# Optimization experiments

Measured on AMD Instinct MI355X. Metric: run time of the kernel, lower is better.

## Reference

```python
import jax, jax.numpy as jnp
import numpy as np

B, CIN, COUT, K, IH, IW = 2, 32, 32, 9, 256, 256
OH, OW = 512, 512


def setup_inputs() -> dict:
    key = jax.random.key(0)
    k0, k1, k2, k3 = jax.random.split(key, 4)
    stdv = 1.0 / np.sqrt(CIN * K)
    x = jax.random.normal(k0, (B, CIN, IH, IW), jnp.float32)
    weight = jax.random.uniform(k1, (CIN, COUT, K), jnp.float32, -stdv, stdv)
    bias = jax.random.uniform(k2, (COUT,), jnp.float32, -stdv, stdv)
    # continuous (x, y) coords into the OUTPUT plane; keep strictly inside so x0+1/y0+1 are valid
    sm = jax.random.uniform(k3, (IH, IW, K, 2), jnp.float32)
    scale = jnp.array([(OW - 1) * 0.999, (OH - 1) * 0.999], jnp.float32)
    sample_map = sm * scale
    return {"x": x, "weight": weight, "bias": bias, "sample_map": sample_map, "oh": OH, "ow": OW}


def reference(x, weight, bias, sample_map, oh, ow):
    Bb, Cin, Ih, Iw = x.shape
    Cout = weight.shape[1]
    Kk = weight.shape[2]
    P = Ih * Iw
    xf = x.reshape(Bb, Cin, P)
    # per-kernel-tap weight transform of every input pixel: [B, Cout, K, P]
    contrib = jnp.einsum('bip,iok->bokp', xf, weight)

    sx = sample_map[..., 0].reshape(P, Kk).T  # [K, P] x-coords in output
    sy = sample_map[..., 1].reshape(P, Kk).T  # [K, P] y-coords in output
    x0f = jnp.floor(sx)
    y0f = jnp.floor(sy)
    dx = sx - x0f
    dy = sy - y0f
    x0 = jnp.clip(x0f.astype(jnp.int32), 0, ow - 1)
    y0 = jnp.clip(y0f.astype(jnp.int32), 0, oh - 1)
    x1 = jnp.clip(x0 + 1, 0, ow - 1)
    y1 = jnp.clip(y0 + 1, 0, oh - 1)

    # bilinear splat weights and flat output indices for the 4 corners: [4, K, P]
    w = jnp.stack([(1 - dx) * (1 - dy), dx * (1 - dy), (1 - dx) * dy, dx * dy], 0)
    idx = jnp.stack([y0 * ow + x0, y0 * ow + x1, y1 * ow + x0, y1 * ow + x1], 0)

    vals = contrib[:, :, None, :, :] * w[None, None, :, :, :]  # [B, Cout, 4, K, P]
    out = jnp.zeros((Bb, Cout, oh * ow), vals.dtype).at[:, :, idx].add(vals)
    return out.reshape(Bb, Cout, oh, ow) + bias[None, :, None, None]
```

## Files before the change

### kernel.cpp

```cpp
#include <hip/hip_runtime.h>
#include <hip/hip_fp16.h>

#define CIN 32
#define COUT 32
#define KK 9
#define PIX 65536
#define OH 512
#define OW 512
#define OHOW (OH*OW)
#define NCH 64
#define TW 16
#define TH 4
#define TPX (TW*TH)
#define NTX (OW/TW)
#define NTY (OH/TH)
#define NTILE (NTX*NTY)
#define NBIN NTILE
#define NPK (PIX*KK)
#define NSEG 4
#define SCAP 96
#define CAPT (NSEG*SCAP)

#define OFF_CNT 0
#define OFF_WT  (256*1024)
#define OFF_ENT (512*1024)
#define OFF_CB  (OFF_ENT + (size_t)NBIN*NSEG*SCAP*8)
#define WS_NEED (OFF_CB + (size_t)NPK*NCH*2)

typedef __bf16    bf16x8 __attribute__((ext_vector_type(8)));
typedef _Float16  f16x8  __attribute__((ext_vector_type(8)));
typedef float     f32x4  __attribute__((ext_vector_type(4)));

__device__ __forceinline__ unsigned short f2h(float v)
{
    return __half_as_ushort(__float2half_rn(v));
}

__device__ __forceinline__ void corners(float sx, float sy,
    int& x0, int& y0, int& x1, int& y1, float& dx, float& dy)
{
    const float x0f = floorf(sx), y0f = floorf(sy);
    dx = sx - x0f; dy = sy - y0f;
    x0 = min(max((int)x0f, 0), OW - 1);
    y0 = min(max((int)y0f, 0), OH - 1);
    x1 = min(x0 + 1, OW - 1);
    y1 = min(y0 + 1, OH - 1);
}

__global__ __launch_bounds__(256) void k_init(
    const float* __restrict__ w, __bf16* __restrict__ wth,
    __bf16* __restrict__ wtl, unsigned* __restrict__ cnt)
{
    const int t = blockIdx.x * 256 + threadIdx.x;
    if (t < NSEG * NBIN) cnt[t] = 0;
    if (t < KK * COUT * CIN) {
        const int i = t & 31;
        const int o = (t >> 5) & 31;
        const int k = t >> 10;
        const float v = w[(i * COUT + o) * KK + k];
        const __bf16 h = (__bf16)v;
        wth[t] = h;
        wtl[t] = (__bf16)(v - (float)h);
    }
}

__global__ __launch_bounds__(256, 1) void k_contrib5(
    const float* __restrict__ x, const __bf16* __restrict__ wth,
    const __bf16* __restrict__ wtl, const float* __restrict__ smap,
    unsigned short* __restrict__ cb, unsigned* __restrict__ cnt,
    uint2* __restrict__ ent)
{
    __shared__ __align__(16) unsigned short patch[4][2][16][72];
    const int tid = threadIdx.x, lane = tid & 63;
    const int wu = __builtin_amdgcn_readfirstlane(tid >> 6);
    const int p0 = blockIdx.x * 64;
    const unsigned seg = blockIdx.x & 3;
    const int colp = lane & 15;
    const int q    = lane >> 4;
    const int cig  = q * 8;

    bf16x8 xh[2], xl[2];
    #pragma unroll
    for (int b = 0; b < 2; ++b) {
        const int p = p0 + wu * 16 + colp;
        #pragma unroll
        for (int j = 0; j < 8; ++j) {
            const float v = x[(size_t)(b * 32 + cig + j) * PIX + p];
            const __bf16 h = (__bf16)v;
            xh[b][j] = h;
            xl[b][j] = (__bf16)(v - (float)h);
        }
    }
    bf16x8 wwh[2][2], wwl[2][2];
    #pragma unroll
    for (int oh = 0; oh < 2; ++oh) {
        wwh[0][oh] = *(const bf16x8*)(wth + (oh * 16 + colp) * 32 + cig);
        wwl[0][oh] = *(const bf16x8*)(wtl + (oh * 16 + colp) * 32 + cig);
    }

    unsigned aS[3][4], aA[3][4], aR[3][4], aW[3];
    #pragma unroll
    for (int it = 0; it < 3; ++it) {
        const int idx = tid + it * 256;
        const bool vit = idx < 576;
        const int t = min(p0 * KK + idx, NPK - 1);
        const float sx = smap[2 * t], sy = smap[2 * t + 1];
        int x0, y0, x1, y1; float dx, dy;
        corners(sx, sy, x0, y0, x1, y1, dx, dy);
        const int g0 = x0 >> 4, g1 = x1 >> 4;
        const int t0 = y0 >> 2, t1 = y1 >> 2;
        aW[it] = (unsigned)f2h(dx) | ((unsigned)f2h(dy) << 16);
        const bool dg = (g1 != g0), dt = (t1 != t0);
        const bool cond[4] = { vit, vit && dg, vit && dt, vit && dg && dt };
        const int  tys[4]  = { t0, t0, t1, t1 };
        const int  gss[4]  = { g0, g1, g0, g1 };
        #pragma unroll
        for (int e = 0; e < 4; ++e) {
            unsigned slot = 0xFFFFFFFFu;
            const int bin = tys[e] * 32 + gss[e];
            const unsigned lxb = (unsigned)(x0 - gss[e] * TW + 1);
            const unsigned lyb = (unsigned)(y0 - tys[e] * TH + 1);
            if (cond[e]) slot = atomicAdd(&cnt[seg * NBIN + bin], 1u);
            aS[it][e] = slot;
            aA[it][e] = ((unsigned)bin * NSEG + seg) * SCAP;
            aR[it][e] = (unsigned)t | (lxb << 20) | (lyb << 25);
        }
    }

    const int pxr = lane >> 2, cc = lane & 3;
    #pragma unroll
    for (int k = 0; k < KK; ++k) {
        const int kb = k & 1;
        const int cur = k & 1, nxt = cur ^ 1;
        if (k + 1 < KK) {
            const __bf16* wb = wth + (k + 1) * (COUT * CIN);
            const __bf16* lb = wtl + (k + 1) * (COUT * CIN);
            #pragma unroll
            for (int oh = 0; oh < 2; ++oh) {
                wwh[nxt][oh] = *(const bf16x8*)(wb + (oh * 16 + colp) * 32 + cig);
                wwl[nxt][oh] = *(const bf16x8*)(lb + (oh * 16 + colp) * 32 + cig);
            }
        }
        #pragma unroll
        for (int cg_ = 0; cg_ < 4; ++cg_) {
            const int b = cg_ >> 1, oh = cg_ & 1;
            f32x4 a = {0.f, 0.f, 0.f, 0.f};
            a = __builtin_amdgcn_mfma_f32_16x16x32_bf16(wwh[cur][oh], xh[b], a, 0, 0, 0);
            a = __builtin_amdgcn_mfma_f32_16x16x32_bf16(wwl[cur][oh], xh[b], a, 0, 0, 0);
            a = __builtin_amdgcn_mfma_f32_16x16x32_bf16(wwh[cur][oh], xl[b], a, 0, 0, 0);
            const unsigned d0 = (unsigned)f2h(a[0]) | ((unsigned)f2h(a[1]) << 16);
            const unsigned d1 = (unsigned)f2h(a[2]) | ((unsigned)f2h(a[3]) << 16);
            *(uint2*)&patch[wu][kb][colp][cg_ * 16 + q * 4] = make_uint2(d0, d1);
        }
        const uint4 a0 = *(const uint4*)&patch[wu][kb][pxr][cc * 8];
        const uint4 a1 = *(const uint4*)&patch[wu][kb][pxr][32 + cc * 8];
        unsigned short* dst = cb + (size_t)(p0 + wu * 16 + pxr) * 576 + k * 64 + cc * 8;
        *(uint4*)dst        = a0;
        *(uint4*)(dst + 32) = a1;
    }

    #pragma unroll
    for (int it = 0; it < 3; ++it) {
        #pragma unroll
        for (int e = 0; e < 4; ++e) {
            if (aS[it][e] < SCAP)
                ent[(size_t)aA[it][e] + aS[it][e]] = make_uint2(aR[it][e], aW[it]);
        }
    }
}

#define LOADU(UU, ITb) { \
    _Pragma("unroll") \
    for (int j = 0; j < 16; ++j) { \
        const unsigned idx = (unsigned)((ITb) * 64 + wv * 16 + j); \
        unsigned short v = 0; \
        if (idx < count) \
            v = cb[((size_t)(elist[idx].x & 0xFFFFFu) << 6) + lane]; \
        UU[j] = v; \
    } }

#define BATCH_BODY(ITc, UU) { \
    { uint4* wq = (uint4*)Wb; const uint4 z = make_uint4(0u,0u,0u,0u); \
      wq[tid] = z; wq[tid + 256] = z; } \
    __syncthreads(); \
    { const int eL = tid >> 2, cn = tid & 3; \
      const unsigned idx = (unsigned)((ITc) * 64 + eL); \
      if (idx < count) { \
        const uint2 r = elist[idx]; \
        const int lx = (int)((r.x >> 20) & 31) - 1 + (cn & 1); \
        const int ly = (int)((r.x >> 25) & 7) - 1 + (cn >> 1); \
        if (((unsigned)lx < TW) & ((unsigned)ly < TH)) { \
            const float dx = __half2float(__ushort_as_half((unsigned short)(r.y & 0xFFFF))); \
            const float dy = __half2float(__ushort_as_half((unsigned short)(r.y >> 16))); \
            const float wx = (cn & 1) ? dx : 1.f - dx; \
            const float wy = (cn >> 1) ? dy : 1.f - dy; \
            const int px = ly * TW + lx; \
            Wb[px * 64 + (eL ^ ((px & 7) << 3))] = f2h(wx * wy); \
        } } } \
    { uint4* cvq = (uint4*)Cv; \
      const uint4 pk0 = make_uint4( \
        (unsigned)UU[0]  | ((unsigned)UU[1]  << 16), (unsigned)UU[2]  | ((unsigned)UU[3]  << 16), \
        (unsigned)UU[4]  | ((unsigned)UU[5]  << 16), (unsigned)UU[6]  | ((unsigned)UU[7]  << 16)); \
      const uint4 pk1 = make_uint4( \
        (unsigned)UU[8]  | ((unsigned)UU[9]  << 16), (unsigned)UU[10] | ((unsigned)UU[11] << 16), \
        (unsigned)UU[12] | ((unsigned)UU[13] << 16), (unsigned)UU[14] | ((unsigned)UU[15] << 16)); \
      cvq[lane * 8 + ((wv * 2)     ^ (lane & 7))] = pk0; \
      cvq[lane * 8 + ((wv * 2 + 1) ^ (lane & 7))] = pk1; } \
    __syncthreads(); \
    { const int m = lane & 15, kh = lane >> 4; \
      const int px = wv * 16 + m; \
      const f16x8 af0 = *(const f16x8*)(Wb + px * 64 + ((kh       ^ (px & 7)) << 3)); \
      const f16x8 af1 = *(const f16x8*)(Wb + px * 64 + (((4 + kh) ^ (px & 7)) << 3)); \
      _Pragma("unroll") \
      for (int n = 0; n < 4; ++n) { \
        const int ch = n * 16 + m; \
        const f16x8 bf0 = *(const f16x8*)(Cv + ch * 64 + ((kh       ^ (ch & 7)) << 3)); \
        acc[n] = __builtin_amdgcn_mfma_f32_16x16x32_f16(af0, bf0, acc[n], 0, 0, 0); \
        const f16x8 bf1 = *(const f16x8*)(Cv + ch * 64 + (((4 + kh) ^ (ch & 7)) << 3)); \
        acc[n] = __builtin_amdgcn_mfma_f32_16x16x32_f16(af1, bf1, acc[n], 0, 0, 0); } } \
    __syncthreads(); }

__global__ __launch_bounds__(256) void k_gather(
    const unsigned short* __restrict__ cb, const uint2* __restrict__ ent,
    const unsigned* __restrict__ cnt, const float* __restrict__ bias,
    float* __restrict__ out)
{
    __shared__ __align__(16) unsigned char smem[16640];
    __shared__ __align__(16) uint2 elist[CAPT];
    unsigned short* Wb = (unsigned short*)smem;
    unsigned short* Cv = (unsigned short*)(smem + 8192);
    const int tid = threadIdx.x, lane = tid & 63;
    const int wv = __builtin_amdgcn_readfirstlane(tid >> 6);
    const int bt = blockIdx.x;
    const int tx0 = (bt & 31) * TW;
    const int ty0 = (bt >> 5) * TH;

    const unsigned c0 = min(cnt[0 * NBIN + bt], (unsigned)SCAP);
    const unsigned c1 = min(cnt[1 * NBIN + bt], (unsigned)SCAP);
    const unsigned c2 = min(cnt[2 * NBIN + bt], (unsigned)SCAP);
    const unsigned c3 = min(cnt[3 * NBIN + bt], (unsigned)SCAP);
    const unsigned o1 = c0, o2 = c0 + c1, o3 = o2 + c2;
    const unsigned count = o3 + c3;
    {
        const uint2* e0 = ent + ((size_t)bt * NSEG + 0) * SCAP;
        const uint2* e1 = ent + ((size_t)bt * NSEG + 1) * SCAP;
        const uint2* e2 = ent + ((size_t)bt * NSEG + 2) * SCAP;
        const uint2* e3 = ent + ((size_t)bt * NSEG + 3) * SCAP;
        if ((unsigned)tid < c0) elist[tid]      = e0[tid];
        if ((unsigned)tid < c1) elist[o1 + tid] = e1[tid];
        if ((unsigned)tid < c2) elist[o2 + tid] = e2[tid];
        if ((unsigned)tid < c3) elist[o3 + tid] = e3[tid];
    }
    __syncthreads();

    const int nb = (int)(count + 63) >> 6;

    unsigned short uA[16], uB[16], uC[16], uD[16];
    LOADU(uA, 0); LOADU(uB, 1); LOADU(uC, 2); LOADU(uD, 3);

    f32x4 acc[4] = {{0.f,0.f,0.f,0.f},{0.f,0.f,0.f,0.f},
                    {0.f,0.f,0.f,0.f},{0.f,0.f,0.f,0.f}};

    if (0 < nb) { BATCH_BODY(0, uA); }
    if (1 < nb) { BATCH_BODY(1, uB); }
    if (2 < nb) { BATCH_BODY(2, uC); }
    if (3 < nb) { BATCH_BODY(3, uD); }
    for (int it = 4; it < nb; ++it) {
        unsigned short ut[16];
        LOADU(ut, it);
        BATCH_BODY(it, ut);
    }

    float* stage = (float*)smem;
    #pragma unroll
    for (int n = 0; n < 4; ++n) {
        #pragma unroll
        for (int r = 0; r < 4; ++r)
            stage[(wv * 16 + (lane >> 4) * 4 + r) * 65 + n * 16 + (lane & 15)] = acc[n][r];
    }
    __syncthreads();
    const int py = lane >> 4, pxx = lane & 15;
    const size_t qq = (size_t)(ty0 + py) * OW + tx0 + pxx;
    #pragma unroll
    for (int j = 0; j < 16; ++j) {
        const int c = wv * 16 + j;
        out[(size_t)c * OHOW + qq] = stage[(py * 16 + pxx) * 65 + c] + bias[c & 31];
    }
}

__global__ __launch_bounds__(576) void mtc_scatter_direct(
    const float* __restrict__ x, const float* __restrict__ weight,
    const float* __restrict__ smap, float* __restrict__ acc)
{
    __shared__ float xs[64][68];
    __shared__ float sm[64 * KK * 2];
    const int t = threadIdx.x;
    const int p0 = blockIdx.x * 64;
    if (t < 512) {
        const int pp = t & 63, c0 = t >> 6;
        #pragma unroll
        for (int ch = 0; ch < 8; ++ch) {
            const int c = c0 + ch * 8;
            xs[pp][c] = x[(size_t)c * PIX + p0 + pp];
        }
    }
    for (int i = t; i < 64 * KK * 2; i += 576)
        sm[i] = smap[(size_t)p0 * (KK * 2) + i];
    const int k = t >> 6, lane = t & 63, b = lane >> 5, o = lane & 31;
    float wreg[CIN];
    #pragma unroll
    for (int i = 0; i < CIN; ++i) wreg[i] = weight[(i * COUT + o) * KK + k];
    __syncthreads();
    for (int pp = 0; pp < 64; ++pp) {
        const float sx = sm[(pp * KK + k) * 2], sy = sm[(pp * KK + k) * 2 + 1];
        int x0, y0, x1, y1; float dx, dy;
        corners(sx, sy, x0, y0, x1, y1, dx, dy);
        const float* xrow = &xs[pp][b * 32];
        float cv = 0.f;
        #pragma unroll
        for (int j = 0; j < 8; ++j) {
            const float4 xv = *(const float4*)(xrow + 4 * j);
            cv += xv.x * wreg[4*j] + xv.y * wreg[4*j+1] + xv.z * wreg[4*j+2] + xv.w * wreg[4*j+3];
        }
        const size_t base = (size_t)lane * OHOW;
        atomicAdd(&acc[base + y0 * OW + x0], cv * (1.f - dx) * (1.f - dy));
        atomicAdd(&acc[base + y0 * OW + x1], cv * dx * (1.f - dy));
        atomicAdd(&acc[base + y1 * OW + x0], cv * (1.f - dx) * dy);
        atomicAdd(&acc[base + y1 * OW + x1], cv * dx * dy);
    }
}

__global__ __launch_bounds__(256) void mtc_bias_add(
    float* __restrict__ out, const float* __restrict__ bias)
{
    const size_t i = (size_t)blockIdx.x * 256 + threadIdx.x;
    out[i] += bias[(i >> 18) & 31];
}

extern "C" void kernel_launch(void* const* d_in, const int* in_sizes, int n_in,
                              void* d_out, int out_size, void* d_ws, size_t ws_size,
                              hipStream_t stream) {
    const float* x      = (const float*)d_in[0];
    const float* weight = (const float*)d_in[1];
    const float* bias   = (const float*)d_in[2];
    const float* smap   = (const float*)d_in[3];
    float* out = (float*)d_out;
    char* ws = (char*)d_ws;

    if (ws_size >= WS_NEED) {
        unsigned* cnt = (unsigned*)(ws + OFF_CNT);
        __bf16* wth   = (__bf16*)(ws + OFF_WT);
        __bf16* wtl   = wth + KK * COUT * CIN;
        uint2* ent    = (uint2*)(ws + OFF_ENT);
        unsigned short* cb = (unsigned short*)(ws + OFF_CB);

        k_init<<<64, 256, 0, stream>>>(weight, wth, wtl, cnt);
        k_contrib5<<<PIX / 64, 256, 0, stream>>>(x, wth, wtl, smap, cb, cnt, ent);
        k_gather<<<NTILE, 256, 0, stream>>>(cb, ent, cnt, bias, out);
    } else {
        hipMemsetAsync(out, 0, (size_t)OHOW * NCH * sizeof(float), stream);
        mtc_scatter_direct<<<PIX / 64, 576, 0, stream>>>(x, weight, smap, out);
        mtc_bias_add<<<(OHOW * NCH) / 256, 256, 0, stream>>>(out, bias);
    }
}
```

Measured before the change: 166.9 us.

## Fuse contrib and gather kernels with a grid-wide spin barrier

```diff
diff --git a/kernel.cpp b/kernel.cpp
--- a/kernel.cpp
+++ b/kernel.cpp
@@ -20,8 +20,10 @@
 #define NSEG 4
 #define SCAP 96
 #define CAPT (NSEG*SCAP)
+#define NBLK 1024
 
 #define OFF_CNT 0
+#define OFF_DONE (128*1024)
 #define OFF_WT  (256*1024)
 #define OFF_ENT (512*1024)
 #define OFF_CB  (OFF_ENT + (size_t)NBIN*NSEG*SCAP*8)
@@ -49,9 +51,11 @@
 
 __global__ __launch_bounds__(256) void k_init(
     const float* __restrict__ w, __bf16* __restrict__ wth,
-    __bf16* __restrict__ wtl, unsigned* __restrict__ cnt)
+    __bf16* __restrict__ wtl, unsigned* __restrict__ cnt,
+    unsigned* __restrict__ done)
 {
     const int t = blockIdx.x * 256 + threadIdx.x;
+    if (t == 0) *done = 0;
     if (t < NSEG * NBIN) cnt[t] = 0;
     if (t < KK * COUT * CIN) {
         const int i = t & 31;
@@ -61,111 +65,6 @@
         const __bf16 h = (__bf16)v;
         wth[t] = h;
         wtl[t] = (__bf16)(v - (float)h);
-    }
-}
-
-__global__ __launch_bounds__(256, 1) void k_contrib5(
-    const float* __restrict__ x, const __bf16* __restrict__ wth,
-    const __bf16* __restrict__ wtl, const float* __restrict__ smap,
-    unsigned short* __restrict__ cb, unsigned* __restrict__ cnt,
-    uint2* __restrict__ ent)
-{
-    __shared__ __align__(16) unsigned short patch[4][2][16][72];
-    const int tid = threadIdx.x, lane = tid & 63;
-    const int wu = __builtin_amdgcn_readfirstlane(tid >> 6);
-    const int p0 = blockIdx.x * 64;
-    const unsigned seg = blockIdx.x & 3;
-    const int colp = lane & 15;
-    const int q    = lane >> 4;
-    const int cig  = q * 8;
-
-    bf16x8 xh[2], xl[2];
-    #pragma unroll
-    for (int b = 0; b < 2; ++b) {
-        const int p = p0 + wu * 16 + colp;
-        #pragma unroll
-        for (int j = 0; j < 8; ++j) {
-            const float v = x[(size_t)(b * 32 + cig + j) * PIX + p];
-            const __bf16 h = (__bf16)v;
-            xh[b][j] = h;
-            xl[b][j] = (__bf16)(v - (float)h);
-        }
-    }
-    bf16x8 wwh[2][2], wwl[2][2];
-    #pragma unroll
-    for (int oh = 0; oh < 2; ++oh) {
-        wwh[0][oh] = *(const bf16x8*)(wth + (oh * 16 + colp) * 32 + cig);
-        wwl[0][oh] = *(const bf16x8*)(wtl + (oh * 16 + colp) * 32 + cig);
-    }
-
-    unsigned aS[3][4], aA[3][4], aR[3][4], aW[3];
-    #pragma unroll
-    for (int it = 0; it < 3; ++it) {
-        const int idx = tid + it * 256;
-        const bool vit = idx < 576;
-        const int t = min(p0 * KK + idx, NPK - 1);
-        const float sx = smap[2 * t], sy = smap[2 * t + 1];
-        int x0, y0, x1, y1; float dx, dy;
-        corners(sx, sy, x0, y0, x1, y1, dx, dy);
-        const int g0 = x0 >> 4, g1 = x1 >> 4;
-        const int t0 = y0 >> 2, t1 = y1 >> 2;
-        aW[it] = (unsigned)f2h(dx) | ((unsigned)f2h(dy) << 16);
-        const bool dg = (g1 != g0), dt = (t1 != t0);
-        const bool cond[4] = { vit, vit && dg, vit && dt, vit && dg && dt };
-        const int  tys[4]  = { t0, t0, t1, t1 };
-        const int  gss[4]  = { g0, g1, g0, g1 };
-        #pragma unroll
-        for (int e = 0; e < 4; ++e) {
-            unsigned slot = 0xFFFFFFFFu;
-            const int bin = tys[e] * 32 + gss[e];
-            const unsigned lxb = (unsigned)(x0 - gss[e] * TW + 1);
-            const unsigned lyb = (unsigned)(y0 - tys[e] * TH + 1);
-            if (cond[e]) slot = atomicAdd(&cnt[seg * NBIN + bin], 1u);
-            aS[it][e] = slot;
-            aA[it][e] = ((unsigned)bin * NSEG + seg) * SCAP;
-            aR[it][e] = (unsigned)t | (lxb << 20) | (lyb << 25);
-        }
-    }
-
-    const int pxr = lane >> 2, cc = lane & 3;
-    #pragma unroll
-    for (int k = 0; k < KK; ++k) {
-        const int kb = k & 1;
-        const int cur = k & 1, nxt = cur ^ 1;
-        if (k + 1 < KK) {
-            const __bf16* wb = wth + (k + 1) * (COUT * CIN);
-            const __bf16* lb = wtl + (k + 1) * (COUT * CIN);
-            #pragma unroll
-            for (int oh = 0; oh < 2; ++oh) {
-                wwh[nxt][oh] = *(const bf16x8*)(wb + (oh * 16 + colp) * 32 + cig);
-                wwl[nxt][oh] = *(const bf16x8*)(lb + (oh * 16 + colp) * 32 + cig);
-            }
-        }
-        #pragma unroll
-        for (int cg_ = 0; cg_ < 4; ++cg_) {
-            const int b = cg_ >> 1, oh = cg_ & 1;
-            f32x4 a = {0.f, 0.f, 0.f, 0.f};
-            a = __builtin_amdgcn_mfma_f32_16x16x32_bf16(wwh[cur][oh], xh[b], a, 0, 0, 0);
-            a = __builtin_amdgcn_mfma_f32_16x16x32_bf16(wwl[cur][oh], xh[b], a, 0, 0, 0);
-            a = __builtin_amdgcn_mfma_f32_16x16x32_bf16(wwh[cur][oh], xl[b], a, 0, 0, 0);
-            const unsigned d0 = (unsigned)f2h(a[0]) | ((unsigned)f2h(a[1]) << 16);
-            const unsigned d1 = (unsigned)f2h(a[2]) | ((unsigned)f2h(a[3]) << 16);
-            *(uint2*)&patch[wu][kb][colp][cg_ * 16 + q * 4] = make_uint2(d0, d1);
-        }
-        const uint4 a0 = *(const uint4*)&patch[wu][kb][pxr][cc * 8];
-        const uint4 a1 = *(const uint4*)&patch[wu][kb][pxr][32 + cc * 8];
-        unsigned short* dst = cb + (size_t)(p0 + wu * 16 + pxr) * 576 + k * 64 + cc * 8;
-        *(uint4*)dst        = a0;
-        *(uint4*)(dst + 32) = a1;
-    }
-
-    #pragma unroll
-    for (int it = 0; it < 3; ++it) {
-        #pragma unroll
-        for (int e = 0; e < 4; ++e) {
-            if (aS[it][e] < SCAP)
-                ent[(size_t)aA[it][e] + aS[it][e]] = make_uint2(aR[it][e], aW[it]);
-        }
     }
 }
 
@@ -220,71 +119,193 @@
         acc[n] = __builtin_amdgcn_mfma_f32_16x16x32_f16(af1, bf1, acc[n], 0, 0, 0); } } \
     __syncthreads(); }
 
-__global__ __launch_bounds__(256) void k_gather(
-    const unsigned short* __restrict__ cb, const uint2* __restrict__ ent,
-    const unsigned* __restrict__ cnt, const float* __restrict__ bias,
-    float* __restrict__ out)
-{
-    __shared__ __align__(16) unsigned char smem[16640];
-    __shared__ __align__(16) uint2 elist[CAPT];
-    unsigned short* Wb = (unsigned short*)smem;
-    unsigned short* Cv = (unsigned short*)(smem + 8192);
+__global__ __launch_bounds__(256, 4) void k_fused(
+    const float* __restrict__ x, const __bf16* __restrict__ wth,
+    const __bf16* __restrict__ wtl, const float* __restrict__ smap,
+    unsigned short* __restrict__ cb, unsigned* __restrict__ cnt,
+    uint2* __restrict__ ent, const float* __restrict__ bias,
+    float* __restrict__ out, unsigned* __restrict__ done)
+{
+    __shared__ __align__(16) unsigned char sbuf[19712];
     const int tid = threadIdx.x, lane = tid & 63;
-    const int wv = __builtin_amdgcn_readfirstlane(tid >> 6);
-    const int bt = blockIdx.x;
-    const int tx0 = (bt & 31) * TW;
-    const int ty0 = (bt >> 5) * TH;
-
-    const unsigned c0 = min(cnt[0 * NBIN + bt], (unsigned)SCAP);
-    const unsigned c1 = min(cnt[1 * NBIN + bt], (unsigned)SCAP);
-    const unsigned c2 = min(cnt[2 * NBIN + bt], (unsigned)SCAP);
-    const unsigned c3 = min(cnt[3 * NBIN + bt], (unsigned)SCAP);
-    const unsigned o1 = c0, o2 = c0 + c1, o3 = o2 + c2;
-    const unsigned count = o3 + c3;
+    const int wu = __builtin_amdgcn_readfirstlane(tid >> 6);
+    const int wv = wu;
+    const int p0 = blockIdx.x * 64;
+    const unsigned seg = blockIdx.x & 3;
+    const int colp = lane & 15;
+    const int q    = lane >> 4;
+    const int cig  = q * 8;
+
     {
-        const uint2* e0 = ent + ((size_t)bt * NSEG + 0) * SCAP;
-        const uint2* e1 = ent + ((size_t)bt * NSEG + 1) * SCAP;
-        const uint2* e2 = ent + ((size_t)bt * NSEG + 2) * SCAP;
-        const uint2* e3 = ent + ((size_t)bt * NSEG + 3) * SCAP;
-        if ((unsigned)tid < c0) elist[tid]      = e0[tid];
-        if ((unsigned)tid < c1) elist[o1 + tid] = e1[tid];
-        if ((unsigned)tid < c2) elist[o2 + tid] = e2[tid];
-        if ((unsigned)tid < c3) elist[o3 + tid] = e3[tid];
-    }
+        unsigned short (*patch)[16][72] =
+            (unsigned short (*)[16][72])(sbuf + wu * 4608);
+
+        bf16x8 xh[2], xl[2];
+        #pragma unroll
+        for (int b = 0; b < 2; ++b) {
+            const int p = p0 + wu * 16 + colp;
+            #pragma unroll
+            for (int j = 0; j < 8; ++j) {
+                const float v = x[(size_t)(b * 32 + cig + j) * PIX + p];
+                const __bf16 h = (__bf16)v;
+                xh[b][j] = h;
+                xl[b][j] = (__bf16)(v - (float)h);
+            }
+        }
+        bf16x8 wwh[2][2], wwl[2][2];
+        #pragma unroll
+        for (int oh = 0; oh < 2; ++oh) {
+            wwh[0][oh] = *(const bf16x8*)(wth + (oh * 16 + colp) * 32 + cig);
+            wwl[0][oh] = *(const bf16x8*)(wtl + (oh * 16 + colp) * 32 + cig);
+        }
+
+        unsigned aS[3][4], aA[3][4], aR[3][4], aW[3];
+        #pragma unroll
+        for (int it = 0; it < 3; ++it) {
+            const int idx = tid + it * 256;
+            const bool vit = idx < 576;
+            const int t = min(p0 * KK + idx, NPK - 1);
+            const float sx = smap[2 * t], sy = smap[2 * t + 1];
+            int x0, y0, x1, y1; float dx, dy;
+            corners(sx, sy, x0, y0, x1, y1, dx, dy);
+            const int g0 = x0 >> 4, g1 = x1 >> 4;
+            const int t0 = y0 >> 2, t1 = y1 >> 2;
+            aW[it] = (unsigned)f2h(dx) | ((unsigned)f2h(dy) << 16);
+            const bool dg = (g1 != g0), dt = (t1 != t0);
+            const bool cond[4] = { vit, vit && dg, vit && dt, vit && dg && dt };
+            const int  tys[4]  = { t0, t0, t1, t1 };
+            const int  gss[4]  = { g0, g1, g0, g1 };
+            #pragma unroll
+            for (int e = 0; e < 4; ++e) {
+                unsigned slot = 0xFFFFFFFFu;
+                const int bin = tys[e] * 32 + gss[e];
+                const unsigned lxb = (unsigned)(x0 - gss[e] * TW + 1);
+                const unsigned lyb = (unsigned)(y0 - tys[e] * TH + 1);
+                if (cond[e]) slot = atomicAdd(&cnt[seg * NBIN + bin], 1u);
+                aS[it][e] = slot;
+                aA[it][e] = ((unsigned)bin * NSEG + seg) * SCAP;
+                aR[it][e] = (unsigned)t | (lxb << 20) | (lyb << 25);
+            }
+        }
+
+        const int pxr = lane >> 2, cc = lane & 3;
+        #pragma unroll
+        for (int k = 0; k < KK; ++k) {
+            const int kb = k & 1;
+            const int cur = k & 1, nxt = cur ^ 1;
+            if (k + 1 < KK) {
+                const __bf16* wb = wth + (k + 1) * (COUT * CIN);
+                const __bf16* lb = wtl + (k + 1) * (COUT * CIN);
+                #pragma unroll
+                for (int oh = 0; oh < 2; ++oh) {
+                    wwh[nxt][oh] = *(const bf16x8*)(wb + (oh * 16 + colp) * 32 + cig);
+                    wwl[nxt][oh] = *(const bf16x8*)(lb + (oh * 16 + colp) * 32 + cig);
+                }
+            }
+            #pragma unroll
+            for (int cg_ = 0; cg_ < 4; ++cg_) {
+                const int b = cg_ >> 1, oh = cg_ & 1;
+                f32x4 a = {0.f, 0.f, 0.f, 0.f};
+                a = __builtin_amdgcn_mfma_f32_16x16x32_bf16(wwh[cur][oh], xh[b], a, 0, 0, 0);
+                a = __builtin_amdgcn_mfma_f32_16x16x32_bf16(wwl[cur][oh], xh[b], a, 0, 0, 0);
+                a = __builtin_amdgcn_mfma_f32_16x16x32_bf16(wwh[cur][oh], xl[b], a, 0, 0, 0);
+                const unsigned d0 = (unsigned)f2h(a[0]) | ((unsigned)f2h(a[1]) << 16);
+                const unsigned d1 = (unsigned)f2h(a[2]) | ((unsigned)f2h(a[3]) << 16);
+                *(uint2*)&patch[kb][colp][cg_ * 16 + q * 4] = make_uint2(d0, d1);
+            }
+            const uint4 a0 = *(const uint4*)&patch[kb][pxr][cc * 8];
+            const uint4 a1 = *(const uint4*)&patch[kb][pxr][32 + cc * 8];
+            unsigned short* dst = cb + (size_t)(p0 + wu * 16 + pxr) * 576 + k * 64 + cc * 8;
+            *(uint4*)dst        = a0;
+            *(uint4*)(dst + 32) = a1;
+        }
+
+        #pragma unroll
+        for (int it = 0; it < 3; ++it) {
+            #pragma unroll
+            for (int e = 0; e < 4; ++e) {
+                if (aS[it][e] < SCAP)
+                    ent[(size_t)aA[it][e] + aS[it][e]] = make_uint2(aR[it][e], aW[it]);
+            }
+        }
+    }
+
     __syncthreads();
-
-    const int nb = (int)(count + 63) >> 6;
-
-    unsigned short uA[16], uB[16], uC[16], uD[16];
-    LOADU(uA, 0); LOADU(uB, 1); LOADU(uC, 2); LOADU(uD, 3);
-
-    f32x4 acc[4] = {{0.f,0.f,0.f,0.f},{0.f,0.f,0.f,0.f},
-                    {0.f,0.f,0.f,0.f},{0.f,0.f,0.f,0.f}};
-
-    if (0 < nb) { BATCH_BODY(0, uA); }
-    if (1 < nb) { BATCH_BODY(1, uB); }
-    if (2 < nb) { BATCH_BODY(2, uC); }
-    if (3 < nb) { BATCH_BODY(3, uD); }
-    for (int it = 4; it < nb; ++it) {
-        unsigned short ut[16];
-        LOADU(ut, it);
-        BATCH_BODY(it, ut);
-    }
-
-    float* stage = (float*)smem;
-    #pragma unroll
-    for (int n = 0; n < 4; ++n) {
-        #pragma unroll
-        for (int r = 0; r < 4; ++r)
-            stage[(wv * 16 + (lane >> 4) * 4 + r) * 65 + n * 16 + (lane & 15)] = acc[n][r];
+    if (tid == 0) {
+        __threadfence();
+        atomicAdd(done, 1u);
+        unsigned v = 0;
+        for (long tries = 0; tries < (1L << 22); ++tries) {
+            v = __hip_atomic_load(done, __ATOMIC_RELAXED, __HIP_MEMORY_SCOPE_AGENT);
+            if (v >= NBLK) break;
+            __builtin_amdgcn_s_sleep(8);
+        }
+        __threadfence();
     }
     __syncthreads();
-    const int py = lane >> 4, pxx = lane & 15;
-    const size_t qq = (size_t)(ty0 + py) * OW + tx0 + pxx;
-    #pragma unroll
-    for (int j = 0; j < 16; ++j) {
-        const int c = wv * 16 + j;
-        out[(size_t)c * OHOW + qq] = stage[(py * 16 + pxx) * 65 + c] + bias[c & 31];
+
+    unsigned short* Wb = (unsigned short*)sbuf;
+    unsigned short* Cv = (unsigned short*)(sbuf + 8192);
+    uint2* elist = (uint2*)(sbuf + 16640);
+
+    for (int jt = 0; jt < 4; ++jt) {
+        const int bt = (blockIdx.x << 2) | jt;
+        const int tx0 = (bt & 31) * TW;
+        const int ty0 = (bt >> 5) * TH;
+
+        __syncthreads();
+
+        const unsigned c0 = min(cnt[0 * NBIN + bt], (unsigned)SCAP);
+        const unsigned c1 = min(cnt[1 * NBIN + bt], (unsigned)SCAP);
+        const unsigned c2 = min(cnt[2 * NBIN + bt], (unsigned)SCAP);
+        const unsigned c3 = min(cnt[3 * NBIN + bt], (unsigned)SCAP);
+        const unsigned o1 = c0, o2 = c0 + c1, o3 = o2 + c2;
+        const unsigned count = o3 + c3;
+        {
+            const uint2* e0 = ent + ((size_t)bt * NSEG + 0) * SCAP;
+            const uint2* e1 = ent + ((size_t)bt * NSEG + 1) * SCAP;
+            const uint2* e2 = ent + ((size_t)bt * NSEG + 2) * SCAP;
+            const uint2* e3 = ent + ((size_t)bt * NSEG + 3) * SCAP;
+            if ((unsigned)tid < c0) elist[tid]      = e0[tid];
+            if ((unsigned)tid < c1) elist[o1 + tid] = e1[tid];
+            if ((unsigned)tid < c2) elist[o2 + tid] = e2[tid];
+            if ((unsigned)tid < c3) elist[o3 + tid] = e3[tid];
+        }
+        __syncthreads();
+
+        const int nb = (int)(count + 63) >> 6;
+
+        unsigned short uA[16], uB[16], uC[16], uD[16];
+        LOADU(uA, 0); LOADU(uB, 1); LOADU(uC, 2); LOADU(uD, 3);
+
+        f32x4 acc[4] = {{0.f,0.f,0.f,0.f},{0.f,0.f,0.f,0.f},
+                        {0.f,0.f,0.f,0.f},{0.f,0.f,0.f,0.f}};
+
+        if (0 < nb) { BATCH_BODY(0, uA); }
+        if (1 < nb) { BATCH_BODY(1, uB); }
+        if (2 < nb) { BATCH_BODY(2, uC); }
+        if (3 < nb) { BATCH_BODY(3, uD); }
+        for (int it = 4; it < nb; ++it) {
+            unsigned short ut[16];
+            LOADU(ut, it);
+            BATCH_BODY(it, ut);
+        }
+
+        float* stage = (float*)sbuf;
+        #pragma unroll
+        for (int n = 0; n < 4; ++n) {
+            #pragma unroll
+            for (int r = 0; r < 4; ++r)
+                stage[(wv * 16 + (lane >> 4) * 4 + r) * 65 + n * 16 + (lane & 15)] = acc[n][r];
+        }
+        __syncthreads();
+        const int py = lane >> 4, pxx = lane & 15;
+        const size_t qq = (size_t)(ty0 + py) * OW + tx0 + pxx;
+        #pragma unroll
+        for (int j = 0; j < 16; ++j) {
+            const int c = wv * 16 + j;
+            out[(size_t)c * OHOW + qq] = stage[(py * 16 + pxx) * 65 + c] + bias[c & 31];
+        }
     }
 }
 
@@ -348,15 +369,16 @@
     char* ws = (char*)d_ws;
 
     if (ws_size >= WS_NEED) {
-        unsigned* cnt = (unsigned*)(ws + OFF_CNT);
-        __bf16* wth   = (__bf16*)(ws + OFF_WT);
-        __bf16* wtl   = wth + KK * COUT * CIN;
-        uint2* ent    = (uint2*)(ws + OFF_ENT);
+        unsigned* cnt  = (unsigned*)(ws + OFF_CNT);
+        unsigned* done = (unsigned*)(ws + OFF_DONE);
+        __bf16* wth    = (__bf16*)(ws + OFF_WT);
+        __bf16* wtl    = wth + KK * COUT * CIN;
+        uint2* ent     = (uint2*)(ws + OFF_ENT);
         unsigned short* cb = (unsigned short*)(ws + OFF_CB);
 
-        k_init<<<64, 256, 0, stream>>>(weight, wth, wtl, cnt);
-        k_contrib5<<<PIX / 64, 256, 0, stream>>>(x, wth, wtl, smap, cb, cnt, ent);
-        k_gather<<<NTILE, 256, 0, stream>>>(cb, ent, cnt, bias, out);
+        k_init<<<64, 256, 0, stream>>>(weight, wth, wtl, cnt, done);
+        k_fused<<<NBLK, 256, 0, stream>>>(x, wth, wtl, smap, cb, cnt, ent,
+                                          bias, out, done);
     } else {
         hipMemsetAsync(out, 0, (size_t)OHOW * NCH * sizeof(float), stream);
         mtc_scatter_direct<<<PIX / 64, 576, 0, stream>>>(x, weight, smap, out);
```

Result: slower. 344.2 us (+106.2%).
